# Performance work log

Measured on AMD Instinct MI355X. Metric: run time of the kernel, lower is better.

The kernel has to match this reference:

```python
import jax, jax.numpy as jnp
import numpy as np

N_NODES = 50000
N_EDGES = 600000
IN_DIM = 128
HID = 128


def gcn_conv(x, W, b, src, dst, num_nodes):
    """PyG-style GCNConv: add self-loops, symmetric D^-1/2 (A+I) D^-1/2 normalization."""
    xw = x @ W  # [N, H]
    loop = jnp.arange(num_nodes)
    s = jnp.concatenate([src, loop])
    d = jnp.concatenate([dst, loop])
    deg = jax.ops.segment_sum(jnp.ones_like(d, dtype=xw.dtype), d, num_segments=num_nodes)
    dinv = jax.lax.rsqrt(deg)  # deg >= 1 thanks to self-loops
    norm = dinv[s] * dinv[d]  # [E+N]
    msgs = xw[s] * norm[:, None]  # gather + scale, [E+N, H]
    out = jax.ops.segment_sum(msgs, d, num_segments=num_nodes)
    return out + b


def setup_inputs() -> dict:
    key = jax.random.key(0)
    ks = jax.random.split(key, 12)
    sc_in = 1.0 / np.sqrt(IN_DIM)
    sc_h = 1.0 / np.sqrt(HID)
    sc_2h = 1.0 / np.sqrt(2 * HID)
    return {
        "x": jax.random.normal(ks[0], (N_NODES, IN_DIM), jnp.float32),
        "hidden_state": jax.random.normal(ks[1], (N_NODES, HID), jnp.float32),
        "edge_index": jax.random.randint(ks[2], (2, N_EDGES), 0, N_NODES, dtype=jnp.int32),
        "W_in": jax.random.normal(ks[3], (IN_DIM, HID), jnp.float32) * sc_in,
        "b_in": jnp.zeros((HID,), jnp.float32),
        "W_hid": jax.random.normal(ks[4], (HID, HID), jnp.float32) * sc_h,
        "b_hid": jnp.zeros((HID,), jnp.float32),
        "W_z": jax.random.normal(ks[5], (2 * HID, HID), jnp.float32) * sc_2h,
        "b_z": jnp.zeros((HID,), jnp.float32),
        "W_r": jax.random.normal(ks[6], (2 * HID, HID), jnp.float32) * sc_2h,
        "b_r": jnp.zeros((HID,), jnp.float32),
        "W_c": jax.random.normal(ks[7], (2 * HID, HID), jnp.float32) * sc_2h,
        "b_c": jnp.zeros((HID,), jnp.float32),
    }


def reference(x, hidden_state, edge_index, W_in, b_in, W_hid, b_hid, W_z, b_z, W_r, b_r, W_c, b_c):
    src, dst = edge_index[0], edge_index[1]
    n = x.shape[0]
    # two stacked GCN layers (dropout identity in eval mode)
    h1 = jax.nn.relu(gcn_conv(x, W_in, b_in, src, dst, n))
    emb = gcn_conv(h1, W_hid, b_hid, src, dst, n)  # [N, H]
    # GRU-style gating
    combined = jnp.concatenate([emb, hidden_state], axis=1)  # [N, 2H]
    update = jax.nn.sigmoid(combined @ W_z + b_z)
    reset = jax.nn.sigmoid(combined @ W_r + b_r)
    cand_in = jnp.concatenate([emb, reset * hidden_state], axis=1)
    candidate = jnp.tanh(cand_in @ W_c + b_c)
    new_hidden = (1.0 - update) * hidden_state + update * candidate
    return new_hidden
```

## Files before the change

kernel.cpp:

```cpp
#include <hip/hip_runtime.h>
#include <cstdint>
#include <cstddef>

typedef unsigned short u16;
typedef unsigned int   u32;

typedef __bf16 bf8   __attribute__((ext_vector_type(8)));
typedef float  f32x4 __attribute__((ext_vector_type(4)));

__device__ __forceinline__ float b2f(u16 v) {
  union { u32 i; float f; } c; c.i = ((u32)v) << 16; return c.f;
}
__device__ __forceinline__ u16 f2b(float f) {
  union { u32 i; float f; } c; c.f = f;
  u32 x = c.i;
  u32 r = (x + 0x7FFFu + ((x >> 16) & 1u)) >> 16;
  return (u16)r;
}
__device__ __forceinline__ float sigf(float x) { return 1.0f / (1.0f + __expf(-x)); }
__device__ __forceinline__ float tanhfast(float x) { return 2.0f * sigf(2.0f * x) - 1.0f; }

__device__ __forceinline__ bf8 cvt8(const float* __restrict__ p) {
  f32x4 lo = *(const f32x4*)p;
  f32x4 hi = *(const f32x4*)(p + 4);
  union { u16 s[8]; bf8 v; } c;
#pragma unroll
  for (int i = 0; i < 4; ++i) { c.s[i] = f2b(lo[i]); c.s[4 + i] = f2b(hi[i]); }
  return c.v;
}

__device__ __forceinline__ void ld_lds16(const u16* g, u16* l) {
  __builtin_amdgcn_global_load_lds((const __attribute__((address_space(1))) void*)g,
                                   (__attribute__((address_space(3))) void*)l, 16, 0, 0);
}

__global__ __launch_bounds__(256) void k_transpose(
    const float* __restrict__ W0, const float* __restrict__ W1,
    const float* __restrict__ W2, const float* __restrict__ W3,
    const float* __restrict__ W4,
    u16* __restrict__ B0, u16* __restrict__ B1, u16* __restrict__ B2,
    u16* __restrict__ B3, u16* __restrict__ B4) {
  int t = blockIdx.x * 256 + threadIdx.x;
  if (t >= 16384) return;
  const float* in; u16* out; int f;
  if (t < 2048)       { in = W0; out = B0; f = t; }
  else if (t < 4096)  { in = W1; out = B1; f = t - 2048; }
  else if (t < 8192)  { in = W2; out = B2; f = t - 4096; }
  else if (t < 12288) { in = W3; out = B3; f = t - 8192; }
  else                { in = W4; out = B4; f = t - 12288; }
  int ln = f & 15, quad = (f >> 4) & 3, c = (f >> 6) & 7, ks = (f >> 9) & 3, hh = f >> 11;
  int n = c * 16 + ln;
  int k0 = hh * 128 + ks * 32 + quad * 8;
  union { u16 s[8]; uint4 q; } tmp;
#pragma unroll
  for (int j = 0; j < 8; ++j) tmp.s[j] = f2b(in[(size_t)(k0 + j) * 128 + n]);
  *(uint4*)(out + (size_t)f * 8) = tmp.q;
}

__global__ void k_zero(int* __restrict__ p, int n) {
  int i = blockIdx.x * 256 + threadIdx.x; if (i < n) p[i] = 0;
}

__global__ void k_count(const int* __restrict__ dst, int* __restrict__ cnt, int E) {
  int e = blockIdx.x * 256 + threadIdx.x; if (e < E) atomicAdd(&cnt[dst[e]], 1);
}

__global__ __launch_bounds__(256) void k_partial(const int* __restrict__ cnt,
                                                 int* __restrict__ bsum, int n) {
  int i = blockIdx.x * 256 + threadIdx.x;
  int v = (i < n) ? cnt[i] : 0;
  for (int off = 1; off < 64; off <<= 1) v += __shfl_down(v, off, 64);
  __shared__ int ws[4];
  int lane = threadIdx.x & 63, w = threadIdx.x >> 6;
  if (lane == 0) ws[w] = v;
  __syncthreads();
  if (threadIdx.x == 0) bsum[blockIdx.x] = ws[0] + ws[1] + ws[2] + ws[3];
}

__global__ void k_scanb(int* __restrict__ bsum, int nb) {
  __shared__ int sm[256];
  int tid = threadIdx.x;
  int v = (tid < nb) ? bsum[tid] : 0;
  sm[tid] = v; __syncthreads();
  int run = v;
  for (int off = 1; off < 256; off <<= 1) {
    int t = (tid >= off) ? sm[tid - off] : 0;
    __syncthreads();
    run += t; sm[tid] = run;
    __syncthreads();
  }
  if (tid < nb) bsum[tid] = run - v;
}

__global__ __launch_bounds__(256) void k_scatter(const int* __restrict__ cnt,
                                                 const int* __restrict__ bsum,
                                                 int* __restrict__ row_start,
                                                 int* __restrict__ cursor,
                                                 float* __restrict__ dinv, int n, int E) {
  int tid = threadIdx.x;
  int i = blockIdx.x * 256 + tid;
  int v = (i < n) ? cnt[i] : 0;
  int lane = tid & 63, w = tid >> 6;
  int run = v;
  for (int off = 1; off < 64; off <<= 1) {
    int t = __shfl_up(run, (unsigned)off, 64);
    if (lane >= off) run += t;
  }
  __shared__ int wsum[4];
  if (lane == 63) wsum[w] = run;
  __syncthreads();
  int woff = 0;
  for (int j = 0; j < w; ++j) woff += wsum[j];
  int excl = woff + run - v;
  if (i < n) {
    int rs = bsum[blockIdx.x] + excl;
    row_start[i] = rs; cursor[i] = rs;
    dinv[i] = rsqrtf((float)v + 1.0f);
  }
  if (i == 0) row_start[n] = E;
}

__global__ void k_fill(const int* __restrict__ src, const int* __restrict__ dst,
                       int* __restrict__ cursor, int* __restrict__ csr_src, int E) {
  int e = blockIdx.x * 256 + threadIdx.x;
  if (e < E) { int p = atomicAdd(&cursor[dst[e]], 1); csr_src[p] = src[e]; }
}

__global__ __launch_bounds__(256) void k_agg(const u16* __restrict__ y,
                                             const int* __restrict__ row_start,
                                             const int* __restrict__ csr_src,
                                             const float* __restrict__ dinv,
                                             const float* __restrict__ bias,
                                             u16* __restrict__ out, int relu, int N) {
  int wv = (blockIdx.x * 256 + threadIdx.x) >> 6;
  int lane = threadIdx.x & 63;
  if (wv >= N) return;
  const u32* yr = (const u32*)y;
  float di = dinv[wv];
  float bi0 = bias[lane * 2], bi1 = bias[lane * 2 + 1];
  u32 sv = yr[(size_t)wv * 64 + lane];
  float a0 = b2f((u16)(sv & 0xFFFF));
  float a1 = b2f((u16)(sv >> 16));
  int p0 = row_start[wv], p1 = row_start[wv + 1];
  int p = p0;
  while (p + 8 <= p1) {
    int s[8]; u32 v[8];
#pragma unroll
    for (int j = 0; j < 8; ++j) s[j] = csr_src[p + j];
#pragma unroll
    for (int j = 0; j < 8; ++j) v[j] = yr[(size_t)s[j] * 64 + lane];
#pragma unroll
    for (int j = 0; j < 8; ++j) { a0 += b2f((u16)(v[j] & 0xFFFF)); a1 += b2f((u16)(v[j] >> 16)); }
    p += 8;
  }
  if (p + 4 <= p1) {
    int s[4]; u32 v[4];
#pragma unroll
    for (int j = 0; j < 4; ++j) s[j] = csr_src[p + j];
#pragma unroll
    for (int j = 0; j < 4; ++j) v[j] = yr[(size_t)s[j] * 64 + lane];
#pragma unroll
    for (int j = 0; j < 4; ++j) { a0 += b2f((u16)(v[j] & 0xFFFF)); a1 += b2f((u16)(v[j] >> 16)); }
    p += 4;
  }
  while (p < p1) {
    int s = csr_src[p++];
    u32 v = yr[(size_t)s * 64 + lane];
    a0 += b2f((u16)(v & 0xFFFF));
    a1 += b2f((u16)(v >> 16));
  }
  float r0 = di * a0 + bi0;
  float r1 = di * a1 + bi1;
  if (relu) { r0 = fmaxf(r0, 0.0f); r1 = fmaxf(r1, 0.0f); }
  u32 o = (u32)f2b(r0) | ((u32)f2b(r1) << 16);
  ((u32*)out)[(size_t)wv * 64 + lane] = o;
}

template <bool AF>
__global__ __launch_bounds__(256) void k_gemm(
    const void* __restrict__ Av,
    const u16* __restrict__ Bt,
    const float* __restrict__ rowscale,
    u16* __restrict__ outb, int M) {
  __shared__ __align__(16) u16 bs[16384];
  int tid = threadIdx.x;
  int lane = tid & 63, wave = tid >> 6;
  int ln = lane & 15, quad = lane >> 4;
  int rowbase = blockIdx.x * 64 + wave * 16;
  int rowA = rowbase + ln;
  long rA = (rowA < M) ? rowA : (M - 1);

  {
    const u16* g = Bt + wave * 4096 + lane * 8;
    u16* l = bs + wave * 4096;
#pragma unroll
    for (int i = 0; i < 8; ++i) ld_lds16(g + i * 512, l + i * 512);
  }

  bf8 af[4];
#pragma unroll
  for (int ks = 0; ks < 4; ++ks) {
    int kk = ks * 32 + quad * 8;
    if (AF) af[ks] = cvt8((const float*)Av + rA * 128 + kk);
    else    af[ks] = *(const bf8*)((const u16*)Av + rA * 128 + kk);
  }

  f32x4 acc[8];
#pragma unroll
  for (int c = 0; c < 8; ++c) { acc[c][0] = 0.f; acc[c][1] = 0.f; acc[c][2] = 0.f; acc[c][3] = 0.f; }

  __syncthreads();
#pragma unroll
  for (int ks = 0; ks < 4; ++ks) {
#pragma unroll
    for (int c = 0; c < 8; ++c) {
      bf8 bfr = *(const bf8*)(bs + ks * 4096 + c * 512 + lane * 8);
      acc[c] = __builtin_amdgcn_mfma_f32_16x16x32_bf16(af[ks], bfr, acc[c], 0, 0, 0);
    }
  }

  int rb = rowbase + quad * 4;
#pragma unroll
  for (int c = 0; c < 8; ++c) {
    int col = c * 16 + ln;
#pragma unroll
    for (int r = 0; r < 4; ++r) {
      int row = rb + r;
      if (row < M) outb[(size_t)row * 128 + col] = f2b(acc[c][r] * rowscale[row]);
    }
  }
}

__global__ __launch_bounds__(256) void k_gru(
    const u16* __restrict__ emb, const float* __restrict__ h,
    const u16* __restrict__ Btz, const u16* __restrict__ Btr, const u16* __restrict__ Btc,
    const float* __restrict__ bz, const float* __restrict__ br, const float* __restrict__ bc,
    float* __restrict__ out, int M) {
  __shared__ __align__(16) u16 bs[16384];
  __shared__ __align__(16) u16 at[64 * 136];
  int tid = threadIdx.x;
  int lane = tid & 63, wave = tid >> 6;
  int ln = lane & 15, quad = lane >> 4;
  int rowbase = blockIdx.x * 64 + wave * 16;
  int rowA = rowbase + ln;
  long rA = (rowA < M) ? rowA : (M - 1);
  int rb = rowbase + quad * 4;

  auto stage = [&](const u16* Bt, int hh) {
    const u16* g = Bt + hh * 16384 + wave * 4096 + lane * 8;
    u16* l = bs + wave * 4096;
#pragma unroll
    for (int i = 0; i < 8; ++i) ld_lds16(g + i * 512, l + i * 512);
  };
  auto mmE = [&](f32x4 (&acc)[8]) {
    bf8 af[4];
#pragma unroll
    for (int ks = 0; ks < 4; ++ks) af[ks] = *(const bf8*)(emb + rA * 128 + ks * 32 + quad * 8);
#pragma unroll
    for (int ks = 0; ks < 4; ++ks)
#pragma unroll
      for (int c = 0; c < 8; ++c) {
        bf8 bfr = *(const bf8*)(bs + ks * 4096 + c * 512 + lane * 8);
        acc[c] = __builtin_amdgcn_mfma_f32_16x16x32_bf16(af[ks], bfr, acc[c], 0, 0, 0);
      }
  };
  auto mmH = [&](f32x4 (&acc)[8]) {
    bf8 af[4];
#pragma unroll
    for (int ks = 0; ks < 4; ++ks) af[ks] = cvt8(h + rA * 128 + ks * 32 + quad * 8);
#pragma unroll
    for (int ks = 0; ks < 4; ++ks)
#pragma unroll
      for (int c = 0; c < 8; ++c) {
        bf8 bfr = *(const bf8*)(bs + ks * 4096 + c * 512 + lane * 8);
        acc[c] = __builtin_amdgcn_mfma_f32_16x16x32_bf16(af[ks], bfr, acc[c], 0, 0, 0);
      }
  };

  f32x4 accz[8], accr[8];
#pragma unroll
  for (int c = 0; c < 8; ++c) {
    accz[c][0] = 0.f; accz[c][1] = 0.f; accz[c][2] = 0.f; accz[c][3] = 0.f;
    accr[c][0] = 0.f; accr[c][1] = 0.f; accr[c][2] = 0.f; accr[c][3] = 0.f;
  }

  stage(Btz, 0);
  f32x4 hc[8];
#pragma unroll
  for (int c = 0; c < 8; ++c) {
    int col = c * 16 + ln;
#pragma unroll
    for (int r = 0; r < 4; ++r) {
      int row = rb + r;
      hc[c][r] = (row < M) ? h[(size_t)row * 128 + col] : 0.0f;
    }
  }
  __syncthreads(); mmE(accz); __syncthreads();
  stage(Btz, 1); __syncthreads(); mmH(accz); __syncthreads();
  stage(Btr, 0); __syncthreads(); mmE(accr); __syncthreads();
  stage(Btr, 1); __syncthreads(); mmH(accr); __syncthreads();

#pragma unroll
  for (int c = 0; c < 8; ++c) {
    int col = c * 16 + ln;
    float bzc = bz[col], brc = br[col];
#pragma unroll
    for (int r = 0; r < 4; ++r) {
      float uu = sigf(accz[c][r] + bzc);
      float rr = sigf(accr[c][r] + brc);
      accz[c][r] = uu;
      int lrow = wave * 16 + quad * 4 + r;
      at[lrow * 136 + col] = f2b(rr * hc[c][r]);
      accr[c][r] = 0.0f;
    }
  }
  __syncthreads();

  stage(Btc, 0); __syncthreads(); mmE(accr); __syncthreads();
  stage(Btc, 1); __syncthreads();
  {
    bf8 af[4];
#pragma unroll
    for (int ks = 0; ks < 4; ++ks)
      af[ks] = *(const bf8*)(at + (wave * 16 + ln) * 136 + ks * 32 + quad * 8);
#pragma unroll
    for (int ks = 0; ks < 4; ++ks)
#pragma unroll
      for (int c = 0; c < 8; ++c) {
        bf8 bfr = *(const bf8*)(bs + ks * 4096 + c * 512 + lane * 8);
        accr[c] = __builtin_amdgcn_mfma_f32_16x16x32_bf16(af[ks], bfr, accr[c], 0, 0, 0);
      }
  }

#pragma unroll
  for (int c = 0; c < 8; ++c) {
    int col = c * 16 + ln;
    float bcc = bc[col];
#pragma unroll
    for (int r = 0; r < 4; ++r) {
      int row = rb + r;
      if (row < M) {
        float cd = tanhfast(accr[c][r] + bcc);
        float uu = accz[c][r];
        out[(size_t)row * 128 + col] = (1.0f - uu) * hc[c][r] + uu * cd;
      }
    }
  }
}

extern "C" void kernel_launch(void* const* d_in, const int* in_sizes, int n_in,
                              void* d_out, int out_size, void* d_ws, size_t ws_size,
                              hipStream_t stream) {
  const float* x     = (const float*)d_in[0];
  const float* h     = (const float*)d_in[1];
  const int*   ei    = (const int*)d_in[2];
  const float* W_in  = (const float*)d_in[3];
  const float* b_in  = (const float*)d_in[4];
  const float* W_hid = (const float*)d_in[5];
  const float* b_hid = (const float*)d_in[6];
  const float* W_z   = (const float*)d_in[7];
  const float* b_z   = (const float*)d_in[8];
  const float* W_r   = (const float*)d_in[9];
  const float* b_r   = (const float*)d_in[10];
  const float* W_c   = (const float*)d_in[11];
  const float* b_c   = (const float*)d_in[12];

  const int N = in_sizes[0] / 128;
  const int E = in_sizes[2] / 2;
  const int* src = ei;
  const int* dst = ei + E;

  char* p = (char*)d_ws;
  auto carve = [&](size_t bytes) { char* r = p; p += (bytes + 255) & ~(size_t)255; return r; };
  u16* Bt_in   = (u16*)carve((size_t)16384 * 2);
  u16* Bt_hid  = (u16*)carve((size_t)16384 * 2);
  u16* Bt_z    = (u16*)carve((size_t)32768 * 2);
  u16* Bt_r    = (u16*)carve((size_t)32768 * 2);
  u16* Bt_c    = (u16*)carve((size_t)32768 * 2);
  int* cnt       = (int*)carve((size_t)N * 4);
  int* row_start = (int*)carve((size_t)(N + 1) * 4);
  int* cursor    = (int*)carve((size_t)N * 4);
  int* bsum      = (int*)carve(1024);
  int* csr       = (int*)carve((size_t)E * 4);
  float* dinv    = (float*)carve((size_t)N * 4);
  u16* y    = (u16*)carve((size_t)N * 128 * 2);
  u16* h1   = (u16*)carve((size_t)N * 128 * 2);
  u16* emb  = (u16*)carve((size_t)N * 128 * 2);

  int gN = (N + 255) / 256;
  int gE = (E + 255) / 256;
  int nb = gN;
  int gG = (N + 63) / 64;
  int gA = (N + 3) / 4;

  k_transpose<<<64, 256, 0, stream>>>(W_in, W_hid, W_z, W_r, W_c,
                                      Bt_in, Bt_hid, Bt_z, Bt_r, Bt_c);
  k_zero<<<gN, 256, 0, stream>>>(cnt, N);
  k_count<<<gE, 256, 0, stream>>>(dst, cnt, E);
  k_partial<<<nb, 256, 0, stream>>>(cnt, bsum, N);
  k_scanb<<<1, 256, 0, stream>>>(bsum, nb);
  k_scatter<<<nb, 256, 0, stream>>>(cnt, bsum, row_start, cursor, dinv, N, E);
  k_fill<<<gE, 256, 0, stream>>>(src, dst, cursor, csr, E);

  k_gemm<true><<<gG, 256, 0, stream>>>(x, Bt_in, dinv, y, N);
  k_agg<<<gA, 256, 0, stream>>>(y, row_start, csr, dinv, b_in, h1, 1, N);
  k_gemm<false><<<gG, 256, 0, stream>>>(h1, Bt_hid, dinv, y, N);
  k_agg<<<gA, 256, 0, stream>>>(y, row_start, csr, dinv, b_hid, emb, 0, N);
  k_gru<<<gG, 256, 0, stream>>>(emb, h, Bt_z, Bt_r, Bt_c, b_z, b_r, b_c, (float*)d_out, N);
}
```

Baseline: 302.2 us.

## Fuse zeroing into transpose, shuffle-broadcast CSR indices, pair GRU GEMM stages

Merges the count-zeroing kernel into the weight transpose launch to save one kernel launch. The aggregation kernel now loads up to 64 neighbor indices per wave in one coalesced load and broadcasts them with shuffles, which replaces many scalar index loads. The GRU kernel doubles its LDS weight buffer so that two weight halves are staged together. This cuts the number of barrier/stage rounds and lets z and r (and both halves of c) share A-fragment loads. The cost is higher LDS use per block, which may lower occupancy.

```diff
diff --git a/kernel.cpp b/kernel.cpp
--- a/kernel.cpp
+++ b/kernel.cpp
@@ -39,9 +39,14 @@
     const float* __restrict__ W2, const float* __restrict__ W3,
     const float* __restrict__ W4,
     u16* __restrict__ B0, u16* __restrict__ B1, u16* __restrict__ B2,
-    u16* __restrict__ B3, u16* __restrict__ B4) {
+    u16* __restrict__ B3, u16* __restrict__ B4,
+    int* __restrict__ cnt, int N) {
+  if (blockIdx.x >= 64) {
+    int i = (blockIdx.x - 64) * 256 + threadIdx.x;
+    if (i < N) cnt[i] = 0;
+    return;
+  }
   int t = blockIdx.x * 256 + threadIdx.x;
-  if (t >= 16384) return;
   const float* in; u16* out; int f;
   if (t < 2048)       { in = W0; out = B0; f = t; }
   else if (t < 4096)  { in = W1; out = B1; f = t - 2048; }
@@ -55,10 +60,6 @@
 #pragma unroll
   for (int j = 0; j < 8; ++j) tmp.s[j] = f2b(in[(size_t)(k0 + j) * 128 + n]);
   *(uint4*)(out + (size_t)f * 8) = tmp.q;
-}
-
-__global__ void k_zero(int* __restrict__ p, int n) {
-  int i = blockIdx.x * 256 + threadIdx.x; if (i < n) p[i] = 0;
 }
 
 __global__ void k_count(const int* __restrict__ dst, int* __restrict__ cnt, int E) {
@@ -142,29 +143,30 @@
   float a0 = b2f((u16)(sv & 0xFFFF));
   float a1 = b2f((u16)(sv >> 16));
   int p0 = row_start[wv], p1 = row_start[wv + 1];
-  int p = p0;
-  while (p + 8 <= p1) {
+  int deg = p1 - p0;
+  int degc = (deg < 64) ? deg : 64;
+  int myidx = (lane < degc) ? csr_src[p0 + lane] : 0;
+  int nb8 = (degc + 7) >> 3;
+  for (int b = 0; b < nb8; ++b) {
+    int base = b * 8;
     int s[8]; u32 v[8];
 #pragma unroll
-    for (int j = 0; j < 8; ++j) s[j] = csr_src[p + j];
-#pragma unroll
-    for (int j = 0; j < 8; ++j) v[j] = yr[(size_t)s[j] * 64 + lane];
-#pragma unroll
-    for (int j = 0; j < 8; ++j) { a0 += b2f((u16)(v[j] & 0xFFFF)); a1 += b2f((u16)(v[j] >> 16)); }
-    p += 8;
-  }
-  if (p + 4 <= p1) {
-    int s[4]; u32 v[4];
-#pragma unroll
-    for (int j = 0; j < 4; ++j) s[j] = csr_src[p + j];
-#pragma unroll
-    for (int j = 0; j < 4; ++j) v[j] = yr[(size_t)s[j] * 64 + lane];
-#pragma unroll
-    for (int j = 0; j < 4; ++j) { a0 += b2f((u16)(v[j] & 0xFFFF)); a1 += b2f((u16)(v[j] >> 16)); }
-    p += 4;
-  }
-  while (p < p1) {
-    int s = csr_src[p++];
+    for (int k = 0; k < 8; ++k) {
+      int jj = base + k;
+      s[k] = __shfl(myidx, (jj < degc) ? jj : 0, 64);
+    }
+#pragma unroll
+    for (int k = 0; k < 8; ++k) v[k] = yr[(size_t)s[k] * 64 + lane];
+#pragma unroll
+    for (int k = 0; k < 8; ++k) {
+      if (base + k < degc) {
+        a0 += b2f((u16)(v[k] & 0xFFFF));
+        a1 += b2f((u16)(v[k] >> 16));
+      }
+    }
+  }
+  for (int p = p0 + 64; p < p1; ++p) {
+    int s = csr_src[p];
     u32 v = yr[(size_t)s * 64 + lane];
     a0 += b2f((u16)(v & 0xFFFF));
     a1 += b2f((u16)(v >> 16));
@@ -236,8 +238,8 @@
     const u16* __restrict__ Btz, const u16* __restrict__ Btr, const u16* __restrict__ Btc,
     const float* __restrict__ bz, const float* __restrict__ br, const float* __restrict__ bc,
     float* __restrict__ out, int M) {
-  __shared__ __align__(16) u16 bs[16384];
-  __shared__ __align__(16) u16 at[64 * 136];
+  __shared__ __align__(16) u16 bs[32768];
+  __shared__ __align__(16) u16 at[8192];
   int tid = threadIdx.x;
   int lane = tid & 63, wave = tid >> 6;
   int ln = lane & 15, quad = lane >> 4;
@@ -246,36 +248,48 @@
   long rA = (rowA < M) ? rowA : (M - 1);
   int rb = rowbase + quad * 4;
 
-  auto stage = [&](const u16* Bt, int hh) {
-    const u16* g = Bt + hh * 16384 + wave * 4096 + lane * 8;
-    u16* l = bs + wave * 4096;
-#pragma unroll
-    for (int i = 0; i < 8; ++i) ld_lds16(g + i * 512, l + i * 512);
+  auto stage2 = [&](const u16* BtA, int hhA, const u16* BtB, int hhB) {
+    const u16* gA = BtA + hhA * 16384 + wave * 4096 + lane * 8;
+    const u16* gB = BtB + hhB * 16384 + wave * 4096 + lane * 8;
+    u16* lA = bs + wave * 4096;
+    u16* lB = bs + 16384 + wave * 4096;
+#pragma unroll
+    for (int i = 0; i < 8; ++i) { ld_lds16(gA + i * 512, lA + i * 512); }
+#pragma unroll
+    for (int i = 0; i < 8; ++i) { ld_lds16(gB + i * 512, lB + i * 512); }
   };
-  auto mmE = [&](f32x4 (&acc)[8]) {
-    bf8 af[4];
-#pragma unroll
-    for (int ks = 0; ks < 4; ++ks) af[ks] = *(const bf8*)(emb + rA * 128 + ks * 32 + quad * 8);
+  auto mmpair = [&](const bf8 (&af)[4], f32x4 (&acc1)[8], f32x4 (&acc2)[8]) {
 #pragma unroll
     for (int ks = 0; ks < 4; ++ks)
 #pragma unroll
       for (int c = 0; c < 8; ++c) {
-        bf8 bfr = *(const bf8*)(bs + ks * 4096 + c * 512 + lane * 8);
-        acc[c] = __builtin_amdgcn_mfma_f32_16x16x32_bf16(af[ks], bfr, acc[c], 0, 0, 0);
+        bf8 b1 = *(const bf8*)(bs + ks * 4096 + c * 512 + lane * 8);
+        acc1[c] = __builtin_amdgcn_mfma_f32_16x16x32_bf16(af[ks], b1, acc1[c], 0, 0, 0);
+        bf8 b2 = *(const bf8*)(bs + 16384 + ks * 4096 + c * 512 + lane * 8);
+        acc2[c] = __builtin_amdgcn_mfma_f32_16x16x32_bf16(af[ks], b2, acc2[c], 0, 0, 0);
       }
   };
-  auto mmH = [&](f32x4 (&acc)[8]) {
-    bf8 af[4];
-#pragma unroll
-    for (int ks = 0; ks < 4; ++ks) af[ks] = cvt8(h + rA * 128 + ks * 32 + quad * 8);
-#pragma unroll
-    for (int ks = 0; ks < 4; ++ks)
-#pragma unroll
-      for (int c = 0; c < 8; ++c) {
-        bf8 bfr = *(const bf8*)(bs + ks * 4096 + c * 512 + lane * 8);
-        acc[c] = __builtin_amdgcn_mfma_f32_16x16x32_bf16(af[ks], bfr, acc[c], 0, 0, 0);
-      }
-  };
+
+  stage2(Btz, 0, Btr, 0);
+
+  bf8 af_e[4], af_h[4];
+#pragma unroll
+  for (int ks = 0; ks < 4; ++ks)
+    af_e[ks] = *(const bf8*)(emb + rA * 128 + ks * 32 + quad * 8);
+#pragma unroll
+  for (int ks = 0; ks < 4; ++ks)
+    af_h[ks] = cvt8(h + rA * 128 + ks * 32 + quad * 8);
+
+  f32x4 hc[8];
+#pragma unroll
+  for (int c = 0; c < 8; ++c) {
+    int col = c * 16 + ln;
+#pragma unroll
+    for (int r = 0; r < 4; ++r) {
+      int row = rb + r;
+      hc[c][r] = (row < M) ? h[(size_t)row * 128 + col] : 0.0f;
+    }
+  }
 
   f32x4 accz[8], accr[8];
 #pragma unroll
@@ -284,21 +298,12 @@
     accr[c][0] = 0.f; accr[c][1] = 0.f; accr[c][2] = 0.f; accr[c][3] = 0.f;
   }
 
-  stage(Btz, 0);
-  f32x4 hc[8];
-#pragma unroll
-  for (int c = 0; c < 8; ++c) {
-    int col = c * 16 + ln;
-#pragma unroll
-    for (int r = 0; r < 4; ++r) {
-      int row = rb + r;
-      hc[c][r] = (row < M) ? h[(size_t)row * 128 + col] : 0.0f;
-    }
-  }
-  __syncthreads(); mmE(accz); __syncthreads();
-  stage(Btz, 1); __syncthreads(); mmH(accz); __syncthreads();
-  stage(Btr, 0); __syncthreads(); mmE(accr); __syncthreads();
-  stage(Btr, 1); __syncthreads(); mmH(accr); __syncthreads();
+  __syncthreads();
+  mmpair(af_e, accz, accr);
+  __syncthreads();
+  stage2(Btz, 1, Btr, 1);
+  __syncthreads();
+  mmpair(af_h, accz, accr);
 
 #pragma unroll
   for (int c = 0; c < 8; ++c) {
@@ -310,27 +315,26 @@
       float rr = sigf(accr[c][r] + brc);
       accz[c][r] = uu;
       int lrow = wave * 16 + quad * 4 + r;
-      at[lrow * 136 + col] = f2b(rr * hc[c][r]);
+      at[lrow * 128 + col] = f2b(rr * hc[c][r]);
       accr[c][r] = 0.0f;
     }
   }
   __syncthreads();
-
-  stage(Btc, 0); __syncthreads(); mmE(accr); __syncthreads();
-  stage(Btc, 1); __syncthreads();
-  {
-    bf8 af[4];
-#pragma unroll
-    for (int ks = 0; ks < 4; ++ks)
-      af[ks] = *(const bf8*)(at + (wave * 16 + ln) * 136 + ks * 32 + quad * 8);
-#pragma unroll
-    for (int ks = 0; ks < 4; ++ks)
-#pragma unroll
-      for (int c = 0; c < 8; ++c) {
-        bf8 bfr = *(const bf8*)(bs + ks * 4096 + c * 512 + lane * 8);
-        accr[c] = __builtin_amdgcn_mfma_f32_16x16x32_bf16(af[ks], bfr, accr[c], 0, 0, 0);
-      }
-  }
+  stage2(Btc, 0, Btc, 1);
+  bf8 af_at[4];
+#pragma unroll
+  for (int ks = 0; ks < 4; ++ks)
+    af_at[ks] = *(const bf8*)(at + (wave * 16 + ln) * 128 + ks * 32 + quad * 8);
+  __syncthreads();
+#pragma unroll
+  for (int ks = 0; ks < 4; ++ks)
+#pragma unroll
+    for (int c = 0; c < 8; ++c) {
+      bf8 b1 = *(const bf8*)(bs + ks * 4096 + c * 512 + lane * 8);
+      accr[c] = __builtin_amdgcn_mfma_f32_16x16x32_bf16(af_e[ks], b1, accr[c], 0, 0, 0);
+      bf8 b2 = *(const bf8*)(bs + 16384 + ks * 4096 + c * 512 + lane * 8);
+      accr[c] = __builtin_amdgcn_mfma_f32_16x16x32_bf16(af_at[ks], b2, accr[c], 0, 0, 0);
+    }
 
 #pragma unroll
   for (int c = 0; c < 8; ++c) {
@@ -393,9 +397,8 @@
   int gG = (N + 63) / 64;
   int gA = (N + 3) / 4;
 
-  k_transpose<<<64, 256, 0, stream>>>(W_in, W_hid, W_z, W_r, W_c,
-                                      Bt_in, Bt_hid, Bt_z, Bt_r, Bt_c);
-  k_zero<<<gN, 256, 0, stream>>>(cnt, N);
+  k_transpose<<<64 + gN, 256, 0, stream>>>(W_in, W_hid, W_z, W_r, W_c,
+                                           Bt_in, Bt_hid, Bt_z, Bt_r, Bt_c, cnt, N);
   k_count<<<gE, 256, 0, stream>>>(dst, cnt, E);
   k_partial<<<nb, 256, 0, stream>>>(cnt, bsum, N);
   k_scanb<<<1, 256, 0, stream>>>(bsum, nb);
```

After: 298.1 us. Within noise of the previous version (-1.4%).
